# Kernel optimization log

Hardware: AMD Instinct MI355X
Metric: run time of the kernel (lower is better)

## Reference

```python
import jax, jax.numpy as jnp
import numpy as np
import math

B, U, IN, H = 4096, 6, 256, 600
IKS, IVS, NIH = 64, 400, 1           # input attention key/value sizes, heads
CKS, CQS, NCH = 32, 32, 4            # comm attention key/query sizes, heads
CVS = H                              # comm value size forced to hidden_size
K = 4                                # top-k active units


@jax.custom_vjp
def blocked_grad(x, mask):
    return x

def _bg_fwd(x, mask):
    return x, mask

def _bg_bwd(mask, g):
    return (g * mask, jnp.zeros_like(mask))

blocked_grad.defvjp(_bg_fwd, _bg_bwd)


def _gll(x, w):
    # GroupLinearLayer: per-unit bmm, x (B,U,din) @ w (U,din,dout) -> (B,U,dout)
    return jnp.einsum('bud,udo->buo', x, w)


def setup_inputs() -> dict:
    key = jax.random.key(0)
    ks = jax.random.split(key, 16)
    r = lambda i, shape: (0.02 * jax.random.normal(ks[i], shape)).astype(jnp.float32)
    return dict(
        x=jax.random.normal(ks[0], (B, 1, IN), jnp.float32),
        hs=jax.random.normal(ks[1], (B, U, H), jnp.float32),
        Wk=r(2, (IN, NIH * IKS)), bk=jnp.zeros((NIH * IKS,), jnp.float32),
        Wv=r(3, (IN, NIH * IVS)), bv=jnp.zeros((NIH * IVS,), jnp.float32),
        Wq=r(4, (U, H, NIH * IKS)),
        x2h_w=r(5, (U, IVS, 3 * H)), h2h_w=r(6, (U, H, 3 * H)),
        Wq_=r(7, (U, H, NCH * CQS)), Wk_=r(8, (U, H, NCH * CKS)),
        Wv_=r(9, (U, H, NCH * CVS)), Wout=r(10, (U, NCH * CVS, CVS)),
    )


def reference(x, hs, Wk, bk, Wv, bv, Wq, x2h_w, h2h_w, Wq_, Wk_, Wv_, Wout):
    h_old = hs
    # append null input along dim 1 -> (B,2,IN)
    xcat = jnp.concatenate([x, jnp.zeros_like(x)], axis=1)
    # ---- input attention + top-k mask ----
    key_l = (xcat @ Wk + bk).reshape(B, 2, NIH, IKS).transpose(0, 2, 1, 3)   # (B,1,2,ks)
    val_l = (xcat @ Wv + bv).reshape(B, 2, NIH, IVS).mean(axis=2)             # (B,2,vs) mean over heads
    qry_l = _gll(hs, Wq).reshape(B, U, NIH, IKS).transpose(0, 2, 1, 3)        # (B,1,U,ks)
    scores = jnp.einsum('bhuk,bhnk->bhun', qry_l, key_l) / math.sqrt(IKS)
    scores = scores.mean(axis=1)                                               # (B,U,2)
    not_null = scores[:, :, 0]
    _, idx = jax.lax.top_k(not_null, K)                                        # (B,K)
    mask = jnp.zeros((B, U), jnp.float32).at[jnp.arange(B)[:, None], idx].set(1.0)
    probs = jax.nn.softmax(scores, axis=-1)                                    # dropout is identity (eval)
    inputs = jnp.einsum('bun,bnv->buv', probs, val_l) * mask[:, :, None]       # (B,U,vs)
    # ---- GroupGRU cell ----
    gx = _gll(inputs, x2h_w)
    gh = _gll(hs, h2h_w)
    i_r, i_i, i_n = jnp.split(gx, 3, axis=2)
    h_r, h_i, h_n = jnp.split(gh, 3, axis=2)
    rg = jax.nn.sigmoid(i_r + h_r)
    ig = jax.nn.sigmoid(i_i + h_i)
    ng = jnp.tanh(i_n + rg * h_n)
    hs = ng + ig * (hs - ng)
    # ---- communication attention (with blocked_grad) ----
    h_b = blocked_grad(hs, mask[:, :, None])
    q = _gll(h_b, Wq_).reshape(B, U, NCH, CQS).transpose(0, 2, 1, 3)   # (B,4,U,32)
    k = _gll(h_b, Wk_).reshape(B, U, NCH, CKS).transpose(0, 2, 1, 3)
    v = _gll(h_b, Wv_).reshape(B, U, NCH, CVS).transpose(0, 2, 1, 3)   # (B,4,U,600)
    att = jax.nn.softmax(jnp.einsum('bhuk,bhnk->bhun', q, k) / math.sqrt(CKS), axis=-1)
    att = att * mask[:, None, :, None]   # zero rows of inactive query units
    ctx = jnp.einsum('bhun,bhnv->bhuv', att, v).transpose(0, 2, 1, 3).reshape(B, U, NCH * CVS)
    ctx = _gll(ctx, Wout) + h_b
    m = mask[:, :, None]
    return m * ctx + (1.0 - m) * h_old
```

## Files before the change

kernel.cpp:

```cpp
#include <hip/hip_runtime.h>
#include <math.h>

typedef unsigned short u16;
typedef __attribute__((ext_vector_type(8))) short short8;
typedef __attribute__((ext_vector_type(4))) float f32x4;

constexpr int NB   = 4096;
constexpr int NU   = 6;
constexpr int NIN  = 256;
constexpr int NH   = 600;
constexpr int IKS  = 64;
constexpr int IVS  = 400;
constexpr int NCH  = 4;
constexpr int CVS  = 600;
constexpr int KTOP = 4;

constexpr int KVW  = IKS + IVS;
constexpr int QKW  = 256;
constexpr int VW   = NCH * CVS;

constexpr int KGRU = 1024;
constexpr int HOFS = 416;
constexpr int NGATE = 640;
constexpr int KH   = 640;
constexpr int VN   = 2432;
constexpr int BC   = 2048;
constexpr int NCHUNK = NB / BC;

constexpr long OFF_KV   = 0;
constexpr long OFF_QRY  = OFF_KV   + (long)NB * KVW;
constexpr long OFF_C0   = OFF_QRY  + (long)NB * NU * IKS;
constexpr long OFF_C1   = OFF_C0   + (long)NB * NU;
constexpr long OFF_MASK = OFF_C1   + (long)NB * NU;
constexpr long OFF_QK   = OFF_MASK + (long)NB * NU;
constexpr long OFF_ATTW = OFF_QK   + (long)NB * NU * QKW;
constexpr long OFF_HNBF = OFF_ATTW + (long)NB * NCH * NU * NU;
constexpr long OFF_WQK  = OFF_HNBF + (long)NU * NB * KH / 2;
constexpr long OFF_WV   = OFF_WQK  + (long)NU * QKW * KH / 2;
constexpr long OFF_WOUT = OFF_WV   + (long)NU * VN * KH / 2;
constexpr long OFF_WGRU = OFF_WOUT + (long)NU * NGATE * VN / 2;
constexpr long OFF_AGRU = OFF_WGRU + (long)NU * 3 * NGATE * KGRU / 2;
constexpr long OFF_VBUF = OFF_WGRU;

__device__ __forceinline__ u16 f2bf(float f) {
    unsigned int x = __float_as_uint(f);
    x += 0x7FFFu + ((x >> 16) & 1u);
    return (u16)(x >> 16);
}
__device__ __forceinline__ float bf2f(u16 u) {
    return __uint_as_float(((unsigned int)u) << 16);
}
__device__ __forceinline__ void gl_lds16(const u16* g, u16* l) {
    __builtin_amdgcn_global_load_lds(
        (const __attribute__((address_space(1))) void*)g,
        (__attribute__((address_space(3))) void*)l, 16, 0, 0);
}

#define WAITVM_(N) asm volatile("s_waitcnt vmcnt(" #N ")" ::: "memory")
#define WAITVM(N)  WAITVM_(N)
#define WAITLG()   asm volatile("s_waitcnt lgkmcnt(0)" ::: "memory")
#define SBAR()     do { __builtin_amdgcn_sched_barrier(0); \
                        __builtin_amdgcn_s_barrier();      \
                        __builtin_amdgcn_sched_barrier(0); } while (0)

__global__ __launch_bounds__(256)
void wtrans_kernel(const float* __restrict__ src, long s_u, int s_ld, int s_colofs,
                   int Ksrc, int Nsub,
                   u16* __restrict__ dst, long d_u, int d_ld, int d_nofs, int d_kofs,
                   int gdiv, int s_gcol, int d_gnofs)
{
    __shared__ float tile[32][33];
    int z = blockIdx.z;
    int u = z, g = 0;
    if (gdiv > 1) { u = z / gdiv; g = z % gdiv; }
    const int k0 = blockIdx.x * 32, n0 = blockIdx.y * 32;
    const int t  = threadIdx.x;
    const int scol = s_colofs + g * s_gcol;
    const int dnof = d_nofs + g * d_gnofs;
    const float* S = src + (long)u * s_u;
    u16* D = dst + (long)u * d_u;
    #pragma unroll
    for (int r = 0; r < 4; r++) {
        int kk = r * 8 + (t >> 5), nn = t & 31;
        float v = 0.f;
        if (k0 + kk < Ksrc && n0 + nn < Nsub)
            v = S[(long)(k0 + kk) * s_ld + scol + n0 + nn];
        tile[kk][nn] = v;
    }
    __syncthreads();
    #pragma unroll
    for (int r = 0; r < 4; r++) {
        int nn = r * 8 + (t >> 5), kk = t & 31;
        if (n0 + nn < Nsub)
            D[(long)(dnof + n0 + nn) * d_ld + d_kofs + k0 + kk] = f2bf(tile[kk][nn]);
    }
}

__global__ __launch_bounds__(256)
void gemm_kv_kernel(const float* __restrict__ x,
                    const float* __restrict__ Wk, const float* __restrict__ bk,
                    const float* __restrict__ Wv, const float* __restrict__ bv,
                    float* __restrict__ kvout)
{
    const int m0 = blockIdx.x * 64;
    const int n0 = blockIdx.y * 64;
    const int tid = threadIdx.x;
    const int tm = tid / 16, tn = tid % 16;
    constexpr int K = NIN, N = KVW;

    __shared__ __align__(16) float As[32][72];
    __shared__ __align__(16) float Ws[32][68];
    float acc[4][4] = {};

    for (int k0 = 0; k0 < K; k0 += 32) {
        #pragma unroll
        for (int s2 = 0; s2 < 2; s2++) {
            int s = tid * 2 + s2;
            int row = s >> 3, kc = s & 7;
            float4 v = *(const float4*)&x[(long)(m0 + row) * K + k0 + kc * 4];
            As[kc*4+0][row] = v.x; As[kc*4+1][row] = v.y;
            As[kc*4+2][row] = v.z; As[kc*4+3][row] = v.w;
        }
        #pragma unroll
        for (int s2 = 0; s2 < 2; s2++) {
            int s = tid * 2 + s2;
            int kr = s >> 4, c4 = s & 15;
            int cg = n0 + c4 * 4;
            float4 v = {0,0,0,0};
            if (cg < IKS)    v = *(const float4*)&Wk[(long)(k0+kr)*IKS + cg];
            else if (cg < N) v = *(const float4*)&Wv[(long)(k0+kr)*IVS + (cg - IKS)];
            *(float4*)&Ws[kr][c4*4] = v;
        }
        __syncthreads();
        #pragma unroll
        for (int kk = 0; kk < 32; kk++) {
            float4 a4 = *(const float4*)&As[kk][tm*4];
            float4 w4 = *(const float4*)&Ws[kk][tn*4];
            float av[4] = {a4.x,a4.y,a4.z,a4.w}, wv[4] = {w4.x,w4.y,w4.z,w4.w};
            #pragma unroll
            for (int i = 0; i < 4; i++)
                #pragma unroll
                for (int j = 0; j < 4; j++)
                    acc[i][j] = fmaf(av[i], wv[j], acc[i][j]);
        }
        __syncthreads();
    }
    #pragma unroll
    for (int i = 0; i < 4; i++) {
        int row = m0 + tm*4 + i;
        #pragma unroll
        for (int j = 0; j < 4; j++) {
            int cg = n0 + tn*4 + j;
            if (cg < N) {
                float bias = (cg < IKS) ? bk[cg] : bv[cg - IKS];
                kvout[(long)row*N + cg] = acc[i][j] + bias;
            }
        }
    }
}

__global__ __launch_bounds__(256)
void gemm_qry_kernel(const float* __restrict__ A,
                     const float* __restrict__ W,
                     float* __restrict__ C)
{
    const int u  = blockIdx.z;
    const int m0 = blockIdx.x * 64;
    const int tid = threadIdx.x;
    const int tm = tid / 16, tn = tid % 16;
    constexpr int K = NH, N = IKS;
    const long lda = (long)NU * NH;

    __shared__ __align__(16) float As[32][72];
    __shared__ __align__(16) float Ws[32][68];
    const float* Au = A + (long)u * K;
    const float* Wu = W + (long)u * K * N;
    float acc[4][4] = {};

    for (int k0 = 0; k0 < K; k0 += 32) {
        #pragma unroll
        for (int s2 = 0; s2 < 2; s2++) {
            int s = tid * 2 + s2;
            int row = s >> 3, kc = s & 7;
            float4 v = {0,0,0,0};
            if (k0 + kc*4 < K)
                v = *(const float4*)&Au[(long)(m0 + row) * lda + k0 + kc * 4];
            As[kc*4+0][row] = v.x; As[kc*4+1][row] = v.y;
            As[kc*4+2][row] = v.z; As[kc*4+3][row] = v.w;
        }
        #pragma unroll
        for (int s2 = 0; s2 < 2; s2++) {
            int s = tid * 2 + s2;
            int kr = s >> 4, c4 = s & 15;
            float4 v = {0,0,0,0};
            if (k0 + kr < K)
                v = *(const float4*)&Wu[(long)(k0 + kr) * N + c4 * 4];
            *(float4*)&Ws[kr][c4*4] = v;
        }
        __syncthreads();
        #pragma unroll
        for (int kk = 0; kk < 32; kk++) {
            float4 a4 = *(const float4*)&As[kk][tm*4];
            float4 w4 = *(const float4*)&Ws[kk][tn*4];
            float av[4] = {a4.x,a4.y,a4.z,a4.w}, wv[4] = {w4.x,w4.y,w4.z,w4.w};
            #pragma unroll
            for (int i = 0; i < 4; i++)
                #pragma unroll
                for (int j = 0; j < 4; j++)
                    acc[i][j] = fmaf(av[i], wv[j], acc[i][j]);
        }
        __syncthreads();
    }
    #pragma unroll
    for (int i = 0; i < 4; i++) {
        int row = m0 + tm*4 + i;
        #pragma unroll
        for (int j = 0; j < 4; j++) {
            int c = tn*4 + j;
            C[(long)row*(NU*IKS) + (long)u*IKS + c] = acc[i][j];
        }
    }
}

__global__ __launch_bounds__(64)
void score_kernel(const float* __restrict__ qry, const float* __restrict__ kv,
                  const float* __restrict__ bk,
                  float* __restrict__ c0, float* __restrict__ c1,
                  float* __restrict__ maskf)
{
    const int b = blockIdx.x;
    const int t = threadIdx.x;
    __shared__ float s0s[NU], s1s[NU];

    float k0v = kv[(long)b*KVW + t];
    float bkv = bk[t];
    for (int u = 0; u < NU; u++) {
        float q  = qry[((long)b*NU + u)*IKS + t];
        float p0 = q * k0v, p1 = q * bkv;
        #pragma unroll
        for (int off = 32; off > 0; off >>= 1) {
            p0 += __shfl_down(p0, off);
            p1 += __shfl_down(p1, off);
        }
        if (t == 0) { s0s[u] = p0 * 0.125f; s1s[u] = p1 * 0.125f; }
    }
    __syncthreads();
    if (t < NU) {
        int u = t;
        float su = s0s[u];
        int rank = 0;
        #pragma unroll
        for (int j = 0; j < NU; j++) {
            float sj = s0s[j];
            if (sj > su || (sj == su && j < u)) rank++;
        }
        float m = (rank < KTOP) ? 1.0f : 0.0f;
        float a = s0s[u], bb = s1s[u];
        float mx = fmaxf(a, bb);
        float e0 = expf(a - mx), e1 = expf(bb - mx);
        float p0 = e0 / (e0 + e1);
        c0[(long)b*NU + u]    = m * p0;
        c1[(long)b*NU + u]    = m * (1.0f - p0);
        maskf[(long)b*NU + u] = m;
    }
}

__global__ __launch_bounds__(256)
void prep_gruA_kernel(const float* __restrict__ kv, const float* __restrict__ bv,
                      const float* __restrict__ hs,
                      const float* __restrict__ c0, const float* __restrict__ c1,
                      u16* __restrict__ Ag)
{
    long id = (long)blockIdx.x * 256 + threadIdx.x;
    const long total = (long)NU * NB * (KGRU / 8);
    if (id >= total) return;
    int k8 = (int)(id % (KGRU / 8));
    int b  = (int)((id / (KGRU / 8)) % NB);
    int u  = (int)(id / ((long)(KGRU / 8) * NB));
    int k  = k8 * 8;
    u16 o[8];
    if (k < IVS) {
        float cv0 = c0[(long)b*NU + u], cv1 = c1[(long)b*NU + u];
        const float* kp = kv + (long)b*KVW + IKS + k;
        const float* bp = bv + k;
        #pragma unroll
        for (int i = 0; i < 8; i++) o[i] = f2bf(cv0*kp[i] + cv1*bp[i]);
    } else if (k >= HOFS && k < HOFS + NH) {
        const float* hp = hs + ((long)b*NU + u)*NH + (k - HOFS);
        #pragma unroll
        for (int i = 0; i < 8; i++) o[i] = f2bf(hp[i]);
    } else {
        #pragma unroll
        for (int i = 0; i < 8; i++) o[i] = 0;
    }
    *(short8*)&Ag[id * 8] = *(const short8*)o;
}

__global__ __launch_bounds__(256, 3)
void gru_mfma_kernel(const u16* __restrict__ Ag, const u16* __restrict__ Wg,
                     const float* __restrict__ hs, u16* __restrict__ hnbf)
{
    const int u  = blockIdx.z;
    const int m0 = blockIdx.x * 128;
    const int n0 = blockIdx.y * 32;
    const int tid = threadIdx.x;
    const int wid = tid >> 6, lane = tid & 63;
    const int wm = wid >> 1, wn = wid & 1;
    const int lrow = lane & 15, lkq = lane >> 4;
    const int srow = lane >> 2;
    const int scs  = (((lane & 3) ^ ((lane >> 3) & 3)) * 8);
    const int cofs = ((lkq ^ ((lrow >> 1) & 3)) * 8);

    __shared__ __align__(16) u16 As[3][128 * 32];
    __shared__ __align__(16) u16 Bs[3][128 * 32];

    const u16* Au = Ag + (long)u * NB * KGRU;
    const u16* Wu = Wg + (long)u * 3 * NGATE * KGRU;

    f32x4 aR[4], aI[4], aNX[4], aNH[4];
    #pragma unroll
    for (int m = 0; m < 4; m++) {
        aR[m] = (f32x4){0,0,0,0}; aI[m] = (f32x4){0,0,0,0};
        aNX[m] = (f32x4){0,0,0,0}; aNH[m] = (f32x4){0,0,0,0};
    }

#define GSTAGE(BUF, T) do {                                                   \
        const long kk0 = (long)(T) * 32;                                      \
        _Pragma("unroll")                                                     \
        for (int i2 = 0; i2 < 2; i2++) {                                      \
            int R = wid*32 + i2*16;                                           \
            int row = R + srow;                                               \
            gl_lds16(Au + (long)(m0 + row)*KGRU + kk0 + scs,                  \
                     &As[BUF][R * 32]);                                       \
            int g = row >> 5; if (g > 2) g = 2;     \
            int rn = row & 31;                                                \
            gl_lds16(Wu + ((long)g*NGATE + n0 + rn)*KGRU + kk0 + scs,         \
                     &Bs[BUF][R * 32]);                                       \
        }                                                                     \
    } while (0)

#define GCOMPUTE(BUF, T) do {                                                 \
        __builtin_amdgcn_s_setprio(1);                                        \
        short8 af[4], bR, bI, bN;                                             \
        _Pragma("unroll")                                                     \
        for (int m = 0; m < 4; m++)                                           \
            af[m] = *(const short8*)&As[BUF][(wm*64 + m*16 + lrow)*32 + cofs];\
        {                                                                     \
            int nr = wn*16 + lrow;                                            \
            bR = *(const short8*)&Bs[BUF][(0*32 + nr)*32 + cofs];             \
            bI = *(const short8*)&Bs[BUF][(1*32 + nr)*32 + cofs];             \
            bN = *(const short8*)&Bs[BUF][(2*32 + nr)*32 + cofs];             \
        }                                                                     \
        _Pragma("unroll")                                                     \
        for (int m = 0; m < 4; m++) {                                         \
            aR[m] = __builtin_amdgcn_mfma_f32_16x16x32_bf16(af[m], bR, aR[m], 0, 0, 0); \
            aI[m] = __builtin_amdgcn_mfma_f32_16x16x32_bf16(af[m], bI, aI[m], 0, 0, 0); \
        }                                                                     \
        if ((T) < HOFS/32) {                                                  \
            _Pragma("unroll")                                                 \
            for (int m = 0; m < 4; m++)                                       \
                aNX[m] = __builtin_amdgcn_mfma_f32_16x16x32_bf16(af[m], bN, aNX[m], 0, 0, 0); \
        } else {                                                              \
            _Pragma("unroll")                                                 \
            for (int m = 0; m < 4; m++)                                       \
                aNH[m] = __builtin_amdgcn_mfma_f32_16x16x32_bf16(af[m], bN, aNH[m], 0, 0, 0); \
        }                                                                     \
        __builtin_amdgcn_s_setprio(0);                                        \
    } while (0)

    constexpr int KSTEPS = KGRU / 32;
    GSTAGE(0, 0);
    int bc = 0, bn = 1;
    for (int t = 0; t < KSTEPS - 1; ++t) {
        GSTAGE(bn, t + 1);
        WAITVM(4); SBAR();
        GCOMPUTE(bc, t);
        bc = bn; bn = (bn == 2) ? 0 : bn + 1;
    }
    WAITVM(0); SBAR();
    GCOMPUTE(bc, KSTEPS - 1);
#undef GCOMPUTE
#undef GSTAGE

    #pragma unroll
    for (int m = 0; m < 4; m++) {
        #pragma unroll
        for (int r = 0; r < 4; r++) {
            int row = m0 + wm*64 + m*16 + lkq*4 + r;
            int col = n0 + wn*16 + lrow;
            u16 ov = 0;
            if (col < NH) {
                float rg = 1.0f / (1.0f + expf(-aR[m][r]));
                float ig = 1.0f / (1.0f + expf(-aI[m][r]));
                float ng = tanhf(aNX[m][r] + rg * aNH[m][r]);
                float h  = hs[((long)row*NU + u)*NH + col];
                ov = f2bf(ng + ig * (h - ng));
            }
            hnbf[(long)u*NB*KH + (long)row*KH + col] = ov;
        }
    }
}

template<int EPI>
__global__ __launch_bounds__(256, 2)
void mfgemm_kernel(const u16* __restrict__ A, long sAu, int lda,
                   const u16* __restrict__ Bw, long sBu, int ldb,
                   float* __restrict__ Cf, u16* __restrict__ C16,
                   long sCu, int ldc, int ksteps,
                   const float* __restrict__ maskf,
                   const u16* __restrict__ hnbf,
                   const float* __restrict__ hs,
                   int bbase)
{
    const int u  = blockIdx.z;
    const int m0 = blockIdx.x * 128;
    const int n0 = blockIdx.y * 128;
    const int tid = threadIdx.x;
    const int wid = tid >> 6, lane = tid & 63;
    const int wm = wid >> 1, wn = wid & 1;
    const int lrow = lane & 15, lkq = lane >> 4;
    const int l8 = lane & 7, lr8 = lane >> 3;
    const int rsw = lrow & 7;

    __shared__ __align__(16) u16 As[2][128 * 64];
    __shared__ __align__(16) u16 Bs[2][128 * 64];

    const u16* Au = A + (long)u * sAu;
    const u16* Bu = Bw + (long)u * sBu;

    f32x4 acc[4][4];
    #pragma unroll
    for (int m = 0; m < 4; m++)
        #pragma unroll
        for (int n = 0; n < 4; n++) acc[m][n] = (f32x4){0,0,0,0};

#define MSTAGE(BUF, KS) do {                                                  \
        const long kk0 = (long)(KS) * 64;                                     \
        _Pragma("unroll")                                                     \
        for (int i2 = 0; i2 < 4; i2++) {                                      \
            int rw = i2*32 + wid*8 + lr8;                                     \
            int co = ((l8 ^ (rw & 7)) * 8);                                   \
            gl_lds16(Au + (long)(m0 + rw)*lda + kk0 + co,                     \
                     &As[BUF][(i2*32 + wid*8) * 64]);                         \
            gl_lds16(Bu + (long)(n0 + rw)*ldb + kk0 + co,                     \
                     &Bs[BUF][(i2*32 + wid*8) * 64]);                         \
        }                                                                     \
    } while (0)

#define MCOMPUTE(BUF) do {                                                    \
        __builtin_amdgcn_s_setprio(1);                                        \
        _Pragma("unroll")                                                     \
        for (int ks2 = 0; ks2 < 2; ks2++) {                                   \
            const int cofs = (((ks2*4 + lkq) ^ rsw) * 8);                     \
            short8 af[4], bfr[4];                                             \
            _Pragma("unroll")                                                 \
            for (int m = 0; m < 4; m++)                                       \
                af[m] = *(const short8*)&As[BUF][(wm*64 + m*16 + lrow)*64 + cofs]; \
            _Pragma("unroll")                                                 \
            for (int n = 0; n < 4; n++)                                       \
                bfr[n] = *(const short8*)&Bs[BUF][(wn*64 + n*16 + lrow)*64 + cofs]; \
            _Pragma("unroll")                                                 \
            for (int m = 0; m < 4; m++)                                       \
                _Pragma("unroll")                                             \
                for (int n = 0; n < 4; n++)                                   \
                    acc[m][n] = __builtin_amdgcn_mfma_f32_16x16x32_bf16(af[m], bfr[n], acc[m][n], 0, 0, 0); \
        }                                                                     \
        __builtin_amdgcn_s_setprio(0);                                        \
    } while (0)

#define MPH(BUF, T, W) do {                                                   \
        if ((T) + 1 < ksteps) MSTAGE((BUF)^1, (T)+1);                         \
        WAITVM(W); SBAR();                                                    \
        MCOMPUTE(BUF);                                                        \
        WAITLG(); SBAR();                                                     \
    } while (0)

    MSTAGE(0, 0);
    int t = 0;
    for (; t + 2 < ksteps; t += 2) { MPH(0, t, 8); MPH(1, t+1, 8); }
    if (t + 2 == ksteps) { MPH(0, t, 8); MPH(1, t+1, 0); }
    else                 { MPH(0, t, 0); }
#undef MPH
#undef MCOMPUTE
#undef MSTAGE

    #pragma unroll
    for (int m = 0; m < 4; m++) {
        #pragma unroll
        for (int r = 0; r < 4; r++) {
            int row = m0 + wm*64 + m*16 + lkq*4 + r;
            #pragma unroll
            for (int n = 0; n < 4; n++) {
                int col = n0 + wn*64 + n*16 + lrow;
                float v = acc[m][n][r];
                if (EPI == 0) {
                    Cf[(long)u*sCu + (long)row*ldc + col] = v;
                } else if (EPI == 2) {
                    C16[(long)u*sCu + (long)row*ldc + col] = f2bf(v);
                } else {
                    if (col < NH) {
                        int b = bbase + row;
                        long o = ((long)b*NU + u)*NH + col;
                        float mk = maskf[(long)b*NU + u];
                        float hv = bf2f(hnbf[(long)u*NB*KH + (long)b*KH + col]);
                        Cf[o] = (mk > 0.5f) ? (v + hv) : hs[o];
                    }
                }
            }
        }
    }
}

__global__ __launch_bounds__(64)
void attw_kernel(const float* __restrict__ qk, const float* __restrict__ maskf,
                 float* __restrict__ attw)
{
    const int bh = blockIdx.x;
    const int b = bh / NCH, h = bh % NCH;
    const int t = threadIdx.x;
    __shared__ float lg[NU][NU];

    if (t < NU * NU) {
        int uq = t / NU, un = t % NU;
        const float* qp = qk + ((long)b*NU + uq)*QKW + h*32;
        const float* kp = qk + ((long)b*NU + un)*QKW + 128 + h*32;
        float s = 0;
        #pragma unroll
        for (int i = 0; i < 32; i++) s = fmaf(qp[i], kp[i], s);
        lg[uq][un] = s * 0.17677669529663687f;
    }
    __syncthreads();
    if (t < NU) {
        int uq = t;
        float mx = -1e30f;
        #pragma unroll
        for (int n = 0; n < NU; n++) mx = fmaxf(mx, lg[uq][n]);
        float e[NU], se = 0;
        #pragma unroll
        for (int n = 0; n < NU; n++) { e[n] = expf(lg[uq][n] - mx); se += e[n]; }
        float m = maskf[(long)b*NU + uq];
        float inv = m / se;
        #pragma unroll
        for (int n = 0; n < NU; n++)
            attw[(((long)b*NCH + h)*NU + uq)*NU + n] = e[n] * inv;
    }
}

__global__ __launch_bounds__(256)
void ctx2_kernel(const float* __restrict__ attw, u16* vc, int bbase)
{
    __shared__ float att_s[32][NCH * NU * NU];
    const int c0 = blockIdx.x * 64;
    const int b0 = blockIdx.y * 32;
    const int tid = threadIdx.x;

    for (int i = tid; i < 32 * 144; i += 256) {
        int bl = i / 144, j = i % 144;
        att_s[bl][j] = attw[(long)(bbase + b0 + bl) * 144 + j];
    }
    __syncthreads();

    const int bl = tid >> 3;
    const int c  = c0 + (tid & 7) * 8;
    const long rowbase = (long)(b0 + bl) * NU;

    if (c >= VW) {
        short8 z = {0,0,0,0,0,0,0,0};
        #pragma unroll
        for (int u = 0; u < NU; u++)
            *(short8*)&vc[(rowbase + u) * VN + c] = z;
        return;
    }
    const int h = c / CVS;
    const float* aw = &att_s[bl][h * 36];

    float vf[NU][8];
    #pragma unroll
    for (int n = 0; n < NU; n++) {
        short8 vv = *(const short8*)&vc[(rowbase + n) * VN + c];
        #pragma unroll
        for (int i = 0; i < 8; i++) vf[n][i] = bf2f((u16)vv[i]);
    }
    #pragma unroll
    for (int u = 0; u < NU; u++) {
        float acc[8] = {};
        #pragma unroll
        for (int n = 0; n < NU; n++) {
            float a = aw[u * 6 + n];
            #pragma unroll
            for (int i = 0; i < 8; i++) acc[i] = fmaf(a, vf[n][i], acc[i]);
        }
        short8 o;
        #pragma unroll
        for (int i = 0; i < 8; i++) o[i] = (short)f2bf(acc[i]);
        *(short8*)&vc[(rowbase + u) * VN + c] = o;
    }
}

extern "C" void kernel_launch(void* const* d_in, const int* in_sizes, int n_in,
                              void* d_out, int out_size, void* d_ws, size_t ws_size,
                              hipStream_t stream)
{
    const float* x    = (const float*)d_in[0];
    const float* hs   = (const float*)d_in[1];
    const float* Wk   = (const float*)d_in[2];
    const float* bk   = (const float*)d_in[3];
    const float* Wv   = (const float*)d_in[4];
    const float* bv   = (const float*)d_in[5];
    const float* Wq   = (const float*)d_in[6];
    const float* x2h  = (const float*)d_in[7];
    const float* h2h  = (const float*)d_in[8];
    const float* Wq_  = (const float*)d_in[9];
    const float* Wk_  = (const float*)d_in[10];
    const float* Wv_  = (const float*)d_in[11];
    const float* Wout = (const float*)d_in[12];
    float* out = (float*)d_out;
    float* ws  = (float*)d_ws;

    float* kv    = ws + OFF_KV;
    float* qry   = ws + OFF_QRY;
    float* c0b   = ws + OFF_C0;
    float* c1b   = ws + OFF_C1;
    float* maskf = ws + OFF_MASK;
    float* qk    = ws + OFF_QK;
    float* attw  = ws + OFF_ATTW;
    u16*   hnbf  = (u16*)(ws + OFF_HNBF);
    u16*   wqk   = (u16*)(ws + OFF_WQK);
    u16*   wv    = (u16*)(ws + OFF_WV);
    u16*   wout  = (u16*)(ws + OFF_WOUT);
    u16*   wgru  = (u16*)(ws + OFF_WGRU);
    u16*   agru  = (u16*)(ws + OFF_AGRU);
    u16*   vcbuf = (u16*)(ws + OFF_VBUF);

    wtrans_kernel<<<dim3(20, 4, NU), 256, 0, stream>>>(
        Wq_, (long)NH*128, 128, 0, NH, 128, wqk, (long)QKW*KH, KH, 0, 0, 1, 0, 0);
    wtrans_kernel<<<dim3(20, 4, NU), 256, 0, stream>>>(
        Wk_, (long)NH*128, 128, 0, NH, 128, wqk, (long)QKW*KH, KH, 128, 0, 1, 0, 0);
    wtrans_kernel<<<dim3(20, 75, NU), 256, 0, stream>>>(
        Wv_, (long)NH*VW, VW, 0, NH, VW, wv, (long)VN*KH, KH, 0, 0, 1, 0, 0);
    wtrans_kernel<<<dim3(76, 19, NU), 256, 0, stream>>>(
        Wout, (long)VW*NH, NH, 0, VW, NH, wout, (long)NGATE*VN, VN, 0, 0, 1, 0, 0);
    wtrans_kernel<<<dim3(13, 19, NU*3), 256, 0, stream>>>(
        x2h, (long)IVS*3*NH, 3*NH, 0, IVS, NH,
        wgru, (long)3*NGATE*KGRU, KGRU, 0, 0, 3, NH, NGATE);
    wtrans_kernel<<<dim3(19, 19, NU*3), 256, 0, stream>>>(
        h2h, (long)NH*3*NH, 3*NH, 0, NH, NH,
        wgru, (long)3*NGATE*KGRU, KGRU, 0, HOFS, 3, NH, NGATE);

    gemm_kv_kernel<<<dim3(NB/64, (KVW+63)/64), 256, 0, stream>>>(x, Wk, bk, Wv, bv, kv);
    gemm_qry_kernel<<<dim3(NB/64, 1, NU), 256, 0, stream>>>(hs, Wq, qry);
    score_kernel<<<NB, 64, 0, stream>>>(qry, kv, bk, c0b, c1b, maskf);

    {
        long total = (long)NU * NB * (KGRU/8);
        prep_gruA_kernel<<<(unsigned)((total + 255)/256), 256, 0, stream>>>(
            kv, bv, hs, c0b, c1b, agru);
    }
    gru_mfma_kernel<<<dim3(NB/128, NGATE/32, NU), 256, 0, stream>>>(agru, wgru, hs, hnbf);

    mfgemm_kernel<0><<<dim3(NB/128, QKW/128, NU), 256, 0, stream>>>(
        hnbf, (long)NB*KH, KH, wqk, (long)QKW*KH, KH,
        qk, nullptr, (long)QKW, NU*QKW, KH/64, nullptr, nullptr, nullptr, 0);
    attw_kernel<<<NB*NCH, 64, 0, stream>>>(qk, maskf, attw);

    for (int ch = 0; ch < NCHUNK; ch++) {
        mfgemm_kernel<2><<<dim3(BC/128, VN/128, NU), 256, 0, stream>>>(
            hnbf + (long)ch*BC*KH, (long)NB*KH, KH, wv, (long)VN*KH, KH,
            nullptr, vcbuf, (long)VN, NU*VN, KH/64, nullptr, nullptr, nullptr, 0);
        ctx2_kernel<<<dim3(VN/64, BC/32), 256, 0, stream>>>(
            attw, vcbuf, ch*BC);
        mfgemm_kernel<1><<<dim3(BC/128, NGATE/128, NU), 256, 0, stream>>>(
            vcbuf, (long)VN, NU*VN, wout, (long)NGATE*VN, VN,
            out, nullptr, 0, 0, VN/64, maskf, hnbf, hs, ch*BC);
    }
}
```

Before: 695.0 us.

## Fold value projection into GRU input weights to shrink GRU K dimension

After: 705.4 us. Within noise of the previous version (+1.5%).

```diff
diff --git a/kernel.cpp b/kernel.cpp
--- a/kernel.cpp
+++ b/kernel.cpp
@@ -15,20 +15,21 @@
 constexpr int CVS  = 600;
 constexpr int KTOP = 4;
 
-constexpr int KVW  = IKS + IVS;
 constexpr int QKW  = 256;
 constexpr int VW   = NCH * CVS;
 
-constexpr int KGRU = 1024;
-constexpr int HOFS = 416;
+constexpr int KG2   = 896;
+constexpr int HOFS2 = 256;
 constexpr int NGATE = 640;
-constexpr int KH   = 640;
-constexpr int VN   = 2432;
-constexpr int BC   = 2048;
+constexpr int NROWS3= 3 * NGATE;
+constexpr int KXP   = 448;
+constexpr int KH    = 640;
+constexpr int VN    = 2432;
+constexpr int BC    = 2048;
 constexpr int NCHUNK = NB / BC;
 
 constexpr long OFF_KV   = 0;
-constexpr long OFF_QRY  = OFF_KV   + (long)NB * KVW;
+constexpr long OFF_QRY  = OFF_KV   + (long)NB * IKS;
 constexpr long OFF_C0   = OFF_QRY  + (long)NB * NU * IKS;
 constexpr long OFF_C1   = OFF_C0   + (long)NB * NU;
 constexpr long OFF_MASK = OFF_C1   + (long)NB * NU;
@@ -38,9 +39,12 @@
 constexpr long OFF_WQK  = OFF_HNBF + (long)NU * NB * KH / 2;
 constexpr long OFF_WV   = OFF_WQK  + (long)NU * QKW * KH / 2;
 constexpr long OFF_WOUT = OFF_WV   + (long)NU * VN * KH / 2;
-constexpr long OFF_WGRU = OFF_WOUT + (long)NU * NGATE * VN / 2;
-constexpr long OFF_AGRU = OFF_WGRU + (long)NU * 3 * NGATE * KGRU / 2;
-constexpr long OFF_VBUF = OFF_WGRU;
+constexpr long OFF_WVB  = OFF_WOUT + (long)NU * NGATE * VN / 2;
+constexpr long OFF_TVEC = OFF_WVB  + (long)256 * KXP / 2;
+constexpr long OFF_WGRU2= OFF_TVEC + (long)NU * NROWS3;
+constexpr long OFF_AGRU2= OFF_WGRU2+ (long)NU * NROWS3 * KG2/2;
+constexpr long OFF_WGRUX = OFF_AGRU2;
+constexpr long OFF_VBUF  = OFF_WGRU2;
 
 __device__ __forceinline__ u16 f2bf(float f) {
     unsigned int x = __float_as_uint(f);
@@ -97,16 +101,38 @@
 }
 
 __global__ __launch_bounds__(256)
-void gemm_kv_kernel(const float* __restrict__ x,
-                    const float* __restrict__ Wk, const float* __restrict__ bk,
-                    const float* __restrict__ Wv, const float* __restrict__ bv,
-                    float* __restrict__ kvout)
+void wvbcast_kernel(const float* __restrict__ Wv, u16* __restrict__ wvb)
+{
+    int id = blockIdx.x * 256 + threadIdx.x;
+    if (id >= 256 * KXP) return;
+    int j = id / KXP, k = id % KXP;
+    wvb[id] = (k < IVS) ? f2bf(Wv[(long)j * IVS + k]) : (u16)0;
+}
+
+__global__ __launch_bounds__(256)
+void tvec_kernel(const u16* __restrict__ wgx, const float* __restrict__ bv,
+                 float* __restrict__ tvec)
+{
+    int id = blockIdx.x * 256 + threadIdx.x;
+    if (id >= NU * NROWS3) return;
+    const u16* row = wgx + (long)id * KXP;
+    float s = 0;
+    for (int k = 0; k < IVS; k += 8) {
+        short8 v = *(const short8*)&row[k];
+        #pragma unroll
+        for (int i = 0; i < 8; i++) s = fmaf(bf2f((u16)v[i]), bv[k + i], s);
+    }
+    tvec[id] = s;
+}
+
+__global__ __launch_bounds__(256)
+void gemm_k0_kernel(const float* __restrict__ x, const float* __restrict__ Wk,
+                    const float* __restrict__ bk, float* __restrict__ kvout)
 {
     const int m0 = blockIdx.x * 64;
-    const int n0 = blockIdx.y * 64;
     const int tid = threadIdx.x;
     const int tm = tid / 16, tn = tid % 16;
-    constexpr int K = NIN, N = KVW;
+    constexpr int K = NIN, N = IKS;
 
     __shared__ __align__(16) float As[32][72];
     __shared__ __align__(16) float Ws[32][68];
@@ -125,10 +151,7 @@
         for (int s2 = 0; s2 < 2; s2++) {
             int s = tid * 2 + s2;
             int kr = s >> 4, c4 = s & 15;
-            int cg = n0 + c4 * 4;
-            float4 v = {0,0,0,0};
-            if (cg < IKS)    v = *(const float4*)&Wk[(long)(k0+kr)*IKS + cg];
-            else if (cg < N) v = *(const float4*)&Wv[(long)(k0+kr)*IVS + (cg - IKS)];
+            float4 v = *(const float4*)&Wk[(long)(k0 + kr) * N + c4 * 4];
             *(float4*)&Ws[kr][c4*4] = v;
         }
         __syncthreads();
@@ -150,11 +173,8 @@
         int row = m0 + tm*4 + i;
         #pragma unroll
         for (int j = 0; j < 4; j++) {
-            int cg = n0 + tn*4 + j;
-            if (cg < N) {
-                float bias = (cg < IKS) ? bk[cg] : bv[cg - IKS];
-                kvout[(long)row*N + cg] = acc[i][j] + bias;
-            }
+            int c = tn*4 + j;
+            kvout[(long)row*N + c] = acc[i][j] + bk[c];
         }
     }
 }
@@ -232,7 +252,7 @@
     const int t = threadIdx.x;
     __shared__ float s0s[NU], s1s[NU];
 
-    float k0v = kv[(long)b*KVW + t];
+    float k0v = kv[(long)b*IKS + t];
     float bkv = bk[t];
     for (int u = 0; u < NU; u++) {
         float q  = qry[((long)b*NU + u)*IKS + t];
@@ -266,27 +286,24 @@
 }
 
 __global__ __launch_bounds__(256)
-void prep_gruA_kernel(const float* __restrict__ kv, const float* __restrict__ bv,
-                      const float* __restrict__ hs,
-                      const float* __restrict__ c0, const float* __restrict__ c1,
-                      u16* __restrict__ Ag)
+void prep_gruA_kernel(const float* __restrict__ x, const float* __restrict__ hs,
+                      const float* __restrict__ c0, u16* __restrict__ Ag)
 {
     long id = (long)blockIdx.x * 256 + threadIdx.x;
-    const long total = (long)NU * NB * (KGRU / 8);
+    const long total = (long)NU * NB * (KG2 / 8);
     if (id >= total) return;
-    int k8 = (int)(id % (KGRU / 8));
-    int b  = (int)((id / (KGRU / 8)) % NB);
-    int u  = (int)(id / ((long)(KGRU / 8) * NB));
+    int k8 = (int)(id % (KG2 / 8));
+    int b  = (int)((id / (KG2 / 8)) % NB);
+    int u  = (int)(id / ((long)(KG2 / 8) * NB));
     int k  = k8 * 8;
     u16 o[8];
-    if (k < IVS) {
-        float cv0 = c0[(long)b*NU + u], cv1 = c1[(long)b*NU + u];
-        const float* kp = kv + (long)b*KVW + IKS + k;
-        const float* bp = bv + k;
-        #pragma unroll
-        for (int i = 0; i < 8; i++) o[i] = f2bf(cv0*kp[i] + cv1*bp[i]);
-    } else if (k >= HOFS && k < HOFS + NH) {
-        const float* hp = hs + ((long)b*NU + u)*NH + (k - HOFS);
+    if (k < HOFS2) {
+        float cv0 = c0[(long)b*NU + u];
+        const float* xp = x + (long)b*NIN + k;
+        #pragma unroll
+        for (int i = 0; i < 8; i++) o[i] = f2bf(cv0 * xp[i]);
+    } else if (k < HOFS2 + NH) {
+        const float* hp = hs + ((long)b*NU + u)*NH + (k - HOFS2);
         #pragma unroll
         for (int i = 0; i < 8; i++) o[i] = f2bf(hp[i]);
     } else {
@@ -298,6 +315,7 @@
 
 __global__ __launch_bounds__(256, 3)
 void gru_mfma_kernel(const u16* __restrict__ Ag, const u16* __restrict__ Wg,
+                     const float* __restrict__ tvec, const float* __restrict__ maskf,
                      const float* __restrict__ hs, u16* __restrict__ hnbf)
 {
     const int u  = blockIdx.z;
@@ -314,8 +332,8 @@
     __shared__ __align__(16) u16 As[3][128 * 32];
     __shared__ __align__(16) u16 Bs[3][128 * 32];
 
-    const u16* Au = Ag + (long)u * NB * KGRU;
-    const u16* Wu = Wg + (long)u * 3 * NGATE * KGRU;
+    const u16* Au = Ag + (long)u * NB * KG2;
+    const u16* Wu = Wg + (long)u * NROWS3 * KG2;
 
     f32x4 aR[4], aI[4], aNX[4], aNH[4];
     #pragma unroll
@@ -330,11 +348,11 @@
         for (int i2 = 0; i2 < 2; i2++) {                                      \
             int R = wid*32 + i2*16;                                           \
             int row = R + srow;                                               \
-            gl_lds16(Au + (long)(m0 + row)*KGRU + kk0 + scs,                  \
+            gl_lds16(Au + (long)(m0 + row)*KG2 + kk0 + scs,                   \
                      &As[BUF][R * 32]);                                       \
             int g = row >> 5; if (g > 2) g = 2;     \
             int rn = row & 31;                                                \
-            gl_lds16(Wu + ((long)g*NGATE + n0 + rn)*KGRU + kk0 + scs,         \
+            gl_lds16(Wu + ((long)g*NGATE + n0 + rn)*KG2 + kk0 + scs,          \
                      &Bs[BUF][R * 32]);                                       \
         }                                                                     \
     } while (0)
@@ -356,7 +374,7 @@
             aR[m] = __builtin_amdgcn_mfma_f32_16x16x32_bf16(af[m], bR, aR[m], 0, 0, 0); \
             aI[m] = __builtin_amdgcn_mfma_f32_16x16x32_bf16(af[m], bI, aI[m], 0, 0, 0); \
         }                                                                     \
-        if ((T) < HOFS/32) {                                                  \
+        if ((T) < HOFS2/32) {                                                 \
             _Pragma("unroll")                                                 \
             for (int m = 0; m < 4; m++)                                       \
                 aNX[m] = __builtin_amdgcn_mfma_f32_16x16x32_bf16(af[m], bN, aNX[m], 0, 0, 0); \
@@ -368,7 +386,7 @@
         __builtin_amdgcn_s_setprio(0);                                        \
     } while (0)
 
-    constexpr int KSTEPS = KGRU / 32;
+    constexpr int KSTEPS = KG2 / 32;
     GSTAGE(0, 0);
     int bc = 0, bn = 1;
     for (int t = 0; t < KSTEPS - 1; ++t) {
@@ -382,17 +400,24 @@
 #undef GCOMPUTE
 #undef GSTAGE
 
+    const int col = n0 + wn*16 + lrow;
+    float tR = 0, tI = 0, tN = 0;
+    if (col < NH) {
+        tR = tvec[(long)u*NROWS3 + col];
+        tI = tvec[(long)u*NROWS3 + NGATE + col];
+        tN = tvec[(long)u*NROWS3 + 2*NGATE + col];
+    }
     #pragma unroll
     for (int m = 0; m < 4; m++) {
         #pragma unroll
         for (int r = 0; r < 4; r++) {
             int row = m0 + wm*64 + m*16 + lkq*4 + r;
-            int col = n0 + wn*16 + lrow;
             u16 ov = 0;
             if (col < NH) {
-                float rg = 1.0f / (1.0f + expf(-aR[m][r]));
-                float ig = 1.0f / (1.0f + expf(-aI[m][r]));
-                float ng = tanhf(aNX[m][r] + rg * aNH[m][r]);
+                float mk = maskf[(long)row*NU + u];
+                float rg = 1.0f / (1.0f + expf(-(aR[m][r] + mk*tR)));
+                float ig = 1.0f / (1.0f + expf(-(aI[m][r] + mk*tI)));
+                float ng = tanhf(aNX[m][r] + mk*tN + rg * aNH[m][r]);
                 float h  = hs[((long)row*NU + u)*NH + col];
                 ov = f2bf(ng + ig * (h - ng));
             }
@@ -628,8 +653,11 @@
     u16*   wqk   = (u16*)(ws + OFF_WQK);
     u16*   wv    = (u16*)(ws + OFF_WV);
     u16*   wout  = (u16*)(ws + OFF_WOUT);
-    u16*   wgru  = (u16*)(ws + OFF_WGRU);
-    u16*   agru  = (u16*)(ws + OFF_AGRU);
+    u16*   wvb   = (u16*)(ws + OFF_WVB);
+    float* tvec  = ws + OFF_TVEC;
+    u16*   wgru2 = (u16*)(ws + OFF_WGRU2);
+    u16*   agru2 = (u16*)(ws + OFF_AGRU2);
+    u16*   wgx   = (u16*)(ws + OFF_WGRUX);
     u16*   vcbuf = (u16*)(ws + OFF_VBUF);
 
     wtrans_kernel<<<dim3(20, 4, NU), 256, 0, stream>>>(
@@ -640,23 +668,29 @@
         Wv_, (long)NH*VW, VW, 0, NH, VW, wv, (long)VN*KH, KH, 0, 0, 1, 0, 0);
     wtrans_kernel<<<dim3(76, 19, NU), 256, 0, stream>>>(
         Wout, (long)VW*NH, NH, 0, VW, NH, wout, (long)NGATE*VN, VN, 0, 0, 1, 0, 0);
-    wtrans_kernel<<<dim3(13, 19, NU*3), 256, 0, stream>>>(
+    wtrans_kernel<<<dim3(KXP/32, 19, NU*3), 256, 0, stream>>>(
         x2h, (long)IVS*3*NH, 3*NH, 0, IVS, NH,
-        wgru, (long)3*NGATE*KGRU, KGRU, 0, 0, 3, NH, NGATE);
-    wtrans_kernel<<<dim3(19, 19, NU*3), 256, 0, stream>>>(
+        wgx, (long)NROWS3*KXP, KXP, 0, 0, 3, NH, NGATE);
+    wtrans_kernel<<<dim3(20, 19, NU*3), 256, 0, stream>>>(
         h2h, (long)NH*3*NH, 3*NH, 0, NH, NH,
-        wgru, (long)3*NGATE*KGRU, KGRU, 0, HOFS, 3, NH, NGATE);
-
-    gemm_kv_kernel<<<dim3(NB/64, (KVW+63)/64), 256, 0, stream>>>(x, Wk, bk, Wv, bv, kv);
+        wgru2, (long)NROWS3*KG2, KG2, 0, HOFS2, 3, NH, NGATE);
+    wvbcast_kernel<<<(256*KXP + 255)/256, 256, 0, stream>>>(Wv, wvb);
+    mfgemm_kernel<2><<<dim3(NROWS3/128, 2, NU), 256, 0, stream>>>(
+        wgx, (long)NROWS3*KXP, KXP, wvb, 0L, KXP,
+        nullptr, wgru2, (long)NROWS3*KG2, KG2, KXP/64, nullptr, nullptr, nullptr, 0);
+    tvec_kernel<<<(NU*NROWS3 + 255)/256, 256, 0, stream>>>(wgx, bv, tvec);
+
+    gemm_k0_kernel<<<NB/64, 256, 0, stream>>>(x, Wk, bk, kv);
     gemm_qry_kernel<<<dim3(NB/64, 1, NU), 256, 0, stream>>>(hs, Wq, qry);
     score_kernel<<<NB, 64, 0, stream>>>(qry, kv, bk, c0b, c1b, maskf);
 
     {
-        long total = (long)NU * NB * (KGRU/8);
+        long total = (long)NU * NB * (KG2/8);
         prep_gruA_kernel<<<(unsigned)((total + 255)/256), 256, 0, stream>>>(
-            kv, bv, hs, c0b, c1b, agru);
-    }
-    gru_mfma_kernel<<<dim3(NB/128, NGATE/32, NU), 256, 0, stream>>>(agru, wgru, hs, hnbf);
+            x, hs, c0b, agru2);
+    }
+    gru_mfma_kernel<<<dim3(NB/128, NGATE/32, NU), 256, 0, stream>>>(
+        agru2, wgru2, tvec, maskf, hs, hnbf);
 
     mfgemm_kernel<0><<<dim3(NB/128, QKW/128, NU), 256, 0, stream>>>(
         hnbf, (long)NB*KH, KH, wqk, (long)QKW*KH, KH,
```
